# Performance work log

Hardware: AMD Instinct MI355X
Metric: run time of the kernel (lower is better)

Reference implementation:

```python
import jax, jax.numpy as jnp
import numpy as np

INITIAL_CAPITAL = 500.0
TRANSACTION_COST = 0.0003
TAU = 1.0  # gumbel-softmax temperature
B, S, F = 256, 4096, 64


def setup_inputs() -> dict:
    key = jax.random.key(0)
    ks = jax.random.split(key, 10)
    features = jax.random.normal(ks[0], (B, S, F), dtype=jnp.float32)
    # make columns 1/2 look like vix level / vix change so branches fire
    features = features.at[:, :, 1].set(20.0 + 10.0 * jax.random.uniform(ks[1], (B, S)))
    features = features.at[:, :, 2].set(0.5 * jax.random.normal(ks[2], (B, S)))
    features = features.at[:, :, 3].set(0.01 * jax.random.normal(ks[3], (B, S)))
    return {
        "features": features,
        "feature_weights": jnp.ones((F,), jnp.float32) / F,
        "long_threshold": jnp.float32(0.52),
        "short_threshold": jnp.float32(0.48),
        "base_position_size": jnp.float32(0.8),
        "conviction_scalar": jnp.float32(0.5),
        "vix_impact": jnp.float32(0.2),
        "vix_collapse_threshold": jnp.float32(0.15),
        "vix_spike_threshold": jnp.float32(0.15),
        "gumbel_noise": jax.random.gumbel(ks[4], (S, B, 3), dtype=jnp.float32),
    }


def reference(features, feature_weights, long_threshold, short_threshold,
              base_position_size, conviction_scalar, vix_impact,
              vix_collapse_threshold, vix_spike_threshold, gumbel_noise):
    batch, seq_len, _ = features.shape
    # predictions: sigmoid of feature-weighted sum  [B,S]
    predictions = jax.nn.sigmoid(jnp.einsum('bsf,f->bs', features, feature_weights))
    # time-major per-step inputs [S,B]
    pred_t = predictions.T
    mom_t = features[:, :, 0].T
    vix_t = features[:, :, 1].T
    vch_t = features[:, :, 2].T
    mret_t = features[:, :, 3].T

    def step(carry, x):
        eq, pos = carry  # eq [B], pos [B,3]
        p, v, dv, m, r, g = x
        signal_strength = jnp.abs(p - 0.5) / 0.5
        vix_collapse = (dv < -vix_collapse_threshold) & (v < 30.0)
        vix_spike = (dv > vix_spike_threshold) & (v > 20.0)
        psz = jnp.clip(base_position_size + conviction_scalar * signal_strength, 0.2, 1.0)
        psz = jnp.where(vix_collapse | vix_spike, psz * (1.0 + vix_impact), psz)
        long_pos = ((p >= long_threshold) & (m > 0)) | vix_collapse
        short_pos = ((p <= short_threshold) & (m < 0)) | vix_spike
        logits = jnp.stack([
            jnp.where(long_pos, 1.0, -10.0),
            jnp.where(short_pos, 1.0, -10.0),
            jnp.where(~long_pos & ~short_pos, 1.0, -10.0),
        ], axis=1)  # [B,3]
        probs = jax.nn.softmax((logits + g) / TAU, axis=1)
        strategy_return = psz * (probs[:, 0] - probs[:, 1]) * r
        position_change = jnp.abs(probs - pos).sum(axis=1)
        eq_new = eq * (1.0 + strategy_return - position_change * TRANSACTION_COST)
        return (eq_new, probs), (eq_new, probs, psz)

    eq0 = jnp.full((batch,), INITIAL_CAPITAL, dtype=features.dtype)
    pos0 = jnp.zeros((batch, 3), features.dtype).at[:, 2].set(1.0)
    (_, _), (eq_seq, pos_seq, psz_seq) = jax.lax.scan(
        step, (eq0, pos0), (pred_t, vix_t, vch_t, mom_t, mret_t, gumbel_noise))
    equity = jnp.concatenate([eq0[:, None], eq_seq.T], axis=1)          # [B,S+1]
    positions = jnp.concatenate([pos0[:, None], jnp.swapaxes(pos_seq, 0, 1)], axis=1)  # [B,S+1,3]
    position_sizes = psz_seq[-1]  # last timestep, matching torch loop leak
    return equity, positions, predictions, position_sizes
```

## Files before the change

kernel.cpp:

```cpp
#include <hip/hip_runtime.h>

#define Bn 256
#define Sn 4096
#define Fn 64
#define TCOST 0.0003f
#define INIT_CAP 500.0f

#define EQ_OFF   0
#define POS_OFF  (Bn * (Sn + 1))
#define PRED_OFF (Bn * (Sn + 1) * 4)
#define PSZ_OFF  (PRED_OFF + Bn * Sn)

#define ROWS_PB 64

__global__ __launch_bounds__(256) void trishot_fwd(
    const float* __restrict__ feat,
    const float* __restrict__ w,
    const float* __restrict__ p_lt, const float* __restrict__ p_st,
    const float* __restrict__ p_bps, const float* __restrict__ p_cs,
    const float* __restrict__ p_vi, const float* __restrict__ p_vct,
    const float* __restrict__ p_vst,
    const float* __restrict__ gumbel,
    float* __restrict__ out)
{
    const int tid  = threadIdx.x;
    const int lane = tid & 63;
    const int wave = tid >> 6;
    const int sub  = lane & 15;
    const int grp  = lane >> 4;

    const float LT = *p_lt, ST = *p_st, BPS = *p_bps, CS = *p_cs,
                VI = *p_vi, VCT = *p_vct, VST = *p_vst;

    const float4 wv = ((const float4*)w)[sub];

    const size_t r0 = (size_t)blockIdx.x * ROWS_PB;

#pragma unroll
    for (int pass = 0; pass < ROWS_PB / 16; ++pass) {
        const size_t row = r0 + (size_t)pass * 16 + (size_t)(wave * 4 + grp);
        const float4 fv = ((const float4*)feat)[row * 16 + sub];

        float x = fv.x * wv.x + fv.y * wv.y + fv.z * wv.z + fv.w * wv.w;
        x += __shfl_xor(x, 1);
        x += __shfl_xor(x, 2);
        x += __shfl_xor(x, 4);
        x += __shfl_xor(x, 8);

        if (sub == 0) {
            const int b = (int)(row >> 12);
            const int s = (int)(row & (Sn - 1));

            const float p = 1.0f / (1.0f + __expf(-x));
            const float mom = fv.x, vix = fv.y, dvix = fv.z, mret = fv.w;

            const float ss = fabsf(p - 0.5f) * 2.0f;
            const bool collapse = (dvix < -VCT) && (vix < 30.0f);
            const bool spike    = (dvix >  VST) && (vix > 20.0f);
            float psz = fminf(fmaxf(BPS + CS * ss, 0.2f), 1.0f);
            if (collapse || spike) psz *= (1.0f + VI);

            const bool lp = ((p >= LT) && (mom > 0.0f)) || collapse;
            const bool sp = ((p <= ST) && (mom < 0.0f)) || spike;
            const float l0 = lp ? 1.0f : -10.0f;
            const float l1 = sp ? 1.0f : -10.0f;
            const float l2 = (!lp && !sp) ? 1.0f : -10.0f;

            const float* g = gumbel + ((size_t)s * Bn + b) * 3;
            const float z0 = l0 + g[0], z1 = l1 + g[1], z2 = l2 + g[2];
            const float zm = fmaxf(z0, fmaxf(z1, z2));
            const float e0 = __expf(z0 - zm), e1 = __expf(z1 - zm),
                        e2 = __expf(z2 - zm);
            const float inv = 1.0f / (e0 + e1 + e2);
            const float q0 = e0 * inv, q1 = e1 * inv, q2 = e2 * inv;

            out[PRED_OFF + row] = p;

            const size_t prow = ((size_t)b * (Sn + 1) + s + 1) * 3;
            float* pos = out + POS_OFF;
            pos[prow + 0] = q0;
            pos[prow + 1] = q1;
            pos[prow + 2] = q2;

            out[EQ_OFF + (size_t)b * (Sn + 1) + s + 1] = psz * (q0 - q1) * mret;

            if (s == 0) {
                const size_t p0row = (size_t)b * (Sn + 1) * 3;
                pos[p0row + 0] = 0.0f;
                pos[p0row + 1] = 0.0f;
                pos[p0row + 2] = 1.0f;
            }
            if (s == Sn - 1) {
                out[PSZ_OFF + b] = psz;
            }
        }
    }
}

#define TB  512
#define CHB 8
#define PAD(i) ((i) + ((i) >> 4))

__global__ __launch_bounds__(TB) void trishot_scan(float* __restrict__ out)
{
    const int b = blockIdx.x;
    const int j = threadIdx.x;

    float* eq = out + EQ_OFF + (size_t)b * (Sn + 1);
    const float* pos = out + POS_OFF + (size_t)b * (Sn + 1) * 3;

    __shared__ float sfac[Sn + Sn / 16];
    __shared__ float sc[TB];

    for (int i = j; i < Sn; i += TB) {
        const float a0 = pos[(size_t)i * 3 + 0];
        const float a1 = pos[(size_t)i * 3 + 1];
        const float a2 = pos[(size_t)i * 3 + 2];
        const float c0 = pos[(size_t)(i + 1) * 3 + 0];
        const float c1 = pos[(size_t)(i + 1) * 3 + 1];
        const float c2 = pos[(size_t)(i + 1) * 3 + 2];
        const float pc = fabsf(c0 - a0) + fabsf(c1 - a1) + fabsf(c2 - a2);
        const float rp = eq[i + 1];
        sfac[PAD(i)] = 1.0f + rp - pc * TCOST;
    }
    __syncthreads();

    float f[CHB];
    float lprod = 1.0f;
    const int t0 = j * CHB;
#pragma unroll
    for (int i = 0; i < CHB; ++i) {
        const float v = sfac[PAD(t0 + i)];
        f[i] = v;
        lprod *= v;
    }
    sc[j] = lprod;
    __syncthreads();

#pragma unroll
    for (int off = 1; off < TB; off <<= 1) {
        const float mine  = sc[j];
        const float other = (j >= off) ? sc[j - off] : 1.0f;
        __syncthreads();
        sc[j] = mine * other;
        __syncthreads();
    }

    float eqv = INIT_CAP * ((j > 0) ? sc[j - 1] : 1.0f);
#pragma unroll
    for (int i = 0; i < CHB; ++i) {
        eqv *= f[i];
        sfac[PAD(t0 + i)] = eqv;
    }
    __syncthreads();
    for (int i = j; i < Sn; i += TB) {
        eq[i + 1] = sfac[PAD(i)];
    }
    if (j == 0) eq[0] = INIT_CAP;
}

extern "C" void kernel_launch(void* const* d_in, const int* in_sizes, int n_in,
                              void* d_out, int out_size, void* d_ws, size_t ws_size,
                              hipStream_t stream) {
    const float* feat   = (const float*)d_in[0];
    const float* w      = (const float*)d_in[1];
    const float* lt     = (const float*)d_in[2];
    const float* st     = (const float*)d_in[3];
    const float* bps    = (const float*)d_in[4];
    const float* cs     = (const float*)d_in[5];
    const float* vi     = (const float*)d_in[6];
    const float* vct    = (const float*)d_in[7];
    const float* vst    = (const float*)d_in[8];
    const float* gumbel = (const float*)d_in[9];
    float* out = (float*)d_out;

    trishot_fwd<<<(Bn * Sn) / ROWS_PB, 256, 0, stream>>>(
        feat, w, lt, st, bps, cs, vi, vct, vst, gumbel, out);
    trishot_scan<<<Bn, TB, 0, stream>>>(out);
}
```

Before: 391.3 us.

## Fuse forward pass and equity scan into one per-batch kernel via LDS

Merges the per-timestep forward kernel and the equity scan kernel into a single kernel with one 1024-thread block per batch row. Softmax probabilities and per-step returns are kept in LDS, so the scan no longer re-reads positions and returns from global memory, and one launch is removed. In exchange, the grid shrinks to one block per batch, which limits latency hiding for the feature stream, and equity writes become strided per thread.

```diff
diff --git a/kernel.cpp b/kernel.cpp
--- a/kernel.cpp
+++ b/kernel.cpp
@@ -11,9 +11,13 @@
 #define PRED_OFF (Bn * (Sn + 1) * 4)
 #define PSZ_OFF  (PRED_OFF + Bn * Sn)
 
-#define ROWS_PB 64
+#define TB   1024
+#define CHB  (Sn / TB)
+#define LQ   (Sn + 1)
+#define PADi(i) ((i) + ((i) >> 3))
+#define LQP  (LQ + (LQ >> 3) + 1)
 
-__global__ __launch_bounds__(256) void trishot_fwd(
+__global__ __launch_bounds__(TB) void trishot_fused(
     const float* __restrict__ feat,
     const float* __restrict__ w,
     const float* __restrict__ p_lt, const float* __restrict__ p_st,
@@ -23,22 +27,29 @@
     const float* __restrict__ gumbel,
     float* __restrict__ out)
 {
+    const int b    = blockIdx.x;
     const int tid  = threadIdx.x;
     const int lane = tid & 63;
-    const int wave = tid >> 6;
     const int sub  = lane & 15;
-    const int grp  = lane >> 4;
+    const int gid  = tid >> 4;
+
+    __shared__ float sq0[LQP];
+    __shared__ float sq1[LQP];
+    __shared__ float sq2[LQP];
+    __shared__ float srp[LQP];
+    __shared__ float sc[TB];
 
     const float LT = *p_lt, ST = *p_st, BPS = *p_bps, CS = *p_cs,
                 VI = *p_vi, VCT = *p_vct, VST = *p_vst;
 
     const float4 wv = ((const float4*)w)[sub];
 
-    const size_t r0 = (size_t)blockIdx.x * ROWS_PB;
+    float* pos = out + POS_OFF;
 
-#pragma unroll
-    for (int pass = 0; pass < ROWS_PB / 16; ++pass) {
-        const size_t row = r0 + (size_t)pass * 16 + (size_t)(wave * 4 + grp);
+#pragma unroll 4
+    for (int it = 0; it < Sn / (TB / 16); ++it) {
+        const int s = it * (TB / 16) + gid;
+        const size_t row = (size_t)b * Sn + s;
         const float4 fv = ((const float4*)feat)[row * 16 + sub];
 
         float x = fv.x * wv.x + fv.y * wv.y + fv.z * wv.z + fv.w * wv.w;
@@ -48,9 +59,6 @@
         x += __shfl_xor(x, 8);
 
         if (sub == 0) {
-            const int b = (int)(row >> 12);
-            const int s = (int)(row & (Sn - 1));
-
             const float p = 1.0f / (1.0f + __expf(-x));
             const float mom = fv.x, vix = fv.y, dvix = fv.z, mret = fv.w;
 
@@ -77,86 +85,70 @@
             out[PRED_OFF + row] = p;
 
             const size_t prow = ((size_t)b * (Sn + 1) + s + 1) * 3;
-            float* pos = out + POS_OFF;
             pos[prow + 0] = q0;
             pos[prow + 1] = q1;
             pos[prow + 2] = q2;
 
-            out[EQ_OFF + (size_t)b * (Sn + 1) + s + 1] = psz * (q0 - q1) * mret;
+            sq0[PADi(s + 1)] = q0;
+            sq1[PADi(s + 1)] = q1;
+            sq2[PADi(s + 1)] = q2;
+            srp[PADi(s + 1)] = psz * (q0 - q1) * mret;
 
-            if (s == 0) {
-                const size_t p0row = (size_t)b * (Sn + 1) * 3;
-                pos[p0row + 0] = 0.0f;
-                pos[p0row + 1] = 0.0f;
-                pos[p0row + 2] = 1.0f;
-            }
             if (s == Sn - 1) {
                 out[PSZ_OFF + b] = psz;
             }
         }
     }
-}
 
-#define TB  512
-#define CHB 8
-#define PAD(i) ((i) + ((i) >> 4))
-
-__global__ __launch_bounds__(TB) void trishot_scan(float* __restrict__ out)
-{
-    const int b = blockIdx.x;
-    const int j = threadIdx.x;
-
-    float* eq = out + EQ_OFF + (size_t)b * (Sn + 1);
-    const float* pos = out + POS_OFF + (size_t)b * (Sn + 1) * 3;
-
-    __shared__ float sfac[Sn + Sn / 16];
-    __shared__ float sc[TB];
-
-    for (int i = j; i < Sn; i += TB) {
-        const float a0 = pos[(size_t)i * 3 + 0];
-        const float a1 = pos[(size_t)i * 3 + 1];
-        const float a2 = pos[(size_t)i * 3 + 2];
-        const float c0 = pos[(size_t)(i + 1) * 3 + 0];
-        const float c1 = pos[(size_t)(i + 1) * 3 + 1];
-        const float c2 = pos[(size_t)(i + 1) * 3 + 2];
-        const float pc = fabsf(c0 - a0) + fabsf(c1 - a1) + fabsf(c2 - a2);
-        const float rp = eq[i + 1];
-        sfac[PAD(i)] = 1.0f + rp - pc * TCOST;
+    if (tid == 0) {
+        sq0[PADi(0)] = 0.0f;
+        sq1[PADi(0)] = 0.0f;
+        sq2[PADi(0)] = 1.0f;
+        const size_t p0row = (size_t)b * (Sn + 1) * 3;
+        pos[p0row + 0] = 0.0f;
+        pos[p0row + 1] = 0.0f;
+        pos[p0row + 2] = 1.0f;
+        out[EQ_OFF + (size_t)b * (Sn + 1)] = INIT_CAP;
     }
     __syncthreads();
 
+    const int t0 = tid * CHB;
+    float prev0 = sq0[PADi(t0)];
+    float prev1 = sq1[PADi(t0)];
+    float prev2 = sq2[PADi(t0)];
+
     float f[CHB];
     float lprod = 1.0f;
-    const int t0 = j * CHB;
 #pragma unroll
     for (int i = 0; i < CHB; ++i) {
-        const float v = sfac[PAD(t0 + i)];
-        f[i] = v;
-        lprod *= v;
+        const int s = t0 + i + 1;
+        const float c0 = sq0[PADi(s)], c1 = sq1[PADi(s)], c2 = sq2[PADi(s)];
+        const float pc = fabsf(c0 - prev0) + fabsf(c1 - prev1)
+                       + fabsf(c2 - prev2);
+        const float fac = 1.0f + srp[PADi(s)] - pc * TCOST;
+        f[i] = fac;
+        lprod *= fac;
+        prev0 = c0; prev1 = c1; prev2 = c2;
     }
-    sc[j] = lprod;
+    sc[tid] = lprod;
     __syncthreads();
 
 #pragma unroll
     for (int off = 1; off < TB; off <<= 1) {
-        const float mine  = sc[j];
-        const float other = (j >= off) ? sc[j - off] : 1.0f;
+        const float mine  = sc[tid];
+        const float other = (tid >= off) ? sc[tid - off] : 1.0f;
         __syncthreads();
-        sc[j] = mine * other;
+        sc[tid] = mine * other;
         __syncthreads();
     }
 
-    float eqv = INIT_CAP * ((j > 0) ? sc[j - 1] : 1.0f);
+    float* eq = out + EQ_OFF + (size_t)b * (Sn + 1);
+    float eqv = INIT_CAP * ((tid > 0) ? sc[tid - 1] : 1.0f);
 #pragma unroll
     for (int i = 0; i < CHB; ++i) {
         eqv *= f[i];
-        sfac[PAD(t0 + i)] = eqv;
+        eq[t0 + i + 1] = eqv;
     }
-    __syncthreads();
-    for (int i = j; i < Sn; i += TB) {
-        eq[i + 1] = sfac[PAD(i)];
-    }
-    if (j == 0) eq[0] = INIT_CAP;
 }
 
 extern "C" void kernel_launch(void* const* d_in, const int* in_sizes, int n_in,
@@ -174,7 +166,6 @@
     const float* gumbel = (const float*)d_in[9];
     float* out = (float*)d_out;
 
-    trishot_fwd<<<(Bn * Sn) / ROWS_PB, 256, 0, stream>>>(
+    trishot_fused<<<Bn, TB, 0, stream>>>(
         feat, w, lt, st, bps, cs, vi, vct, vst, gumbel, out);
-    trishot_scan<<<Bn, TB, 0, stream>>>(out);
 }
```

New measurement: 406.0 us. 3.8% more time.

## Replace shared-memory Hillis-Steele scan with wave-shuffle two-level product scan

Applied to the files above, without the earlier changes.

The per-batch cumulative product scan now uses 1024 threads with 4 elements each, doing an intra-wave shuffle scan followed by a small cross-wave scan over 16 wave totals. This replaces a 9-step shared-memory Hillis-Steele scan that needed two barriers per step. Results are written straight from registers to global memory instead of being staged back through shared memory. In exchange, the final stores are strided rather than coalesced, and the padding pattern used for the shared-memory stage changes.

```diff
diff --git a/kernel.cpp b/kernel.cpp
--- a/kernel.cpp
+++ b/kernel.cpp
@@ -97,65 +97,71 @@
     }
 }
 
-#define TB  512
-#define CHB 8
-#define PAD(i) ((i) + ((i) >> 4))
+#define TB   1024
+#define CHB  (Sn / TB)
+#define PADi(i) ((i) + ((i) >> 3))
 
 __global__ __launch_bounds__(TB) void trishot_scan(float* __restrict__ out)
 {
     const int b = blockIdx.x;
     const int j = threadIdx.x;
+    const int lane = j & 63;
+    const int wid  = j >> 6;
 
     float* eq = out + EQ_OFF + (size_t)b * (Sn + 1);
     const float* pos = out + POS_OFF + (size_t)b * (Sn + 1) * 3;
 
-    __shared__ float sfac[Sn + Sn / 16];
-    __shared__ float sc[TB];
+    __shared__ float sfac[Sn + (Sn >> 3)];
+    __shared__ float swave[16];
 
     for (int i = j; i < Sn; i += TB) {
-        const float a0 = pos[(size_t)i * 3 + 0];
-        const float a1 = pos[(size_t)i * 3 + 1];
-        const float a2 = pos[(size_t)i * 3 + 2];
-        const float c0 = pos[(size_t)(i + 1) * 3 + 0];
-        const float c1 = pos[(size_t)(i + 1) * 3 + 1];
-        const float c2 = pos[(size_t)(i + 1) * 3 + 2];
+        const float a0 = pos[i * 3 + 0];
+        const float a1 = pos[i * 3 + 1];
+        const float a2 = pos[i * 3 + 2];
+        const float c0 = pos[i * 3 + 3];
+        const float c1 = pos[i * 3 + 4];
+        const float c2 = pos[i * 3 + 5];
         const float pc = fabsf(c0 - a0) + fabsf(c1 - a1) + fabsf(c2 - a2);
         const float rp = eq[i + 1];
-        sfac[PAD(i)] = 1.0f + rp - pc * TCOST;
+        sfac[PADi(i)] = 1.0f + rp - pc * TCOST;
     }
     __syncthreads();
 
-    float f[CHB];
-    float lprod = 1.0f;
     const int t0 = j * CHB;
+    const float f0 = sfac[PADi(t0 + 0)];
+    const float f1 = sfac[PADi(t0 + 1)];
+    const float f2 = sfac[PADi(t0 + 2)];
+    const float f3 = sfac[PADi(t0 + 3)];
+    const float lprod = f0 * f1 * f2 * f3;
+
+    float incl = lprod;
 #pragma unroll
-    for (int i = 0; i < CHB; ++i) {
-        const float v = sfac[PAD(t0 + i)];
-        f[i] = v;
-        lprod *= v;
+    for (int off = 1; off < 64; off <<= 1) {
+        const float v = __shfl_up(incl, off);
+        if (lane >= off) incl *= v;
     }
-    sc[j] = lprod;
+    if (lane == 63) swave[wid] = incl;
     __syncthreads();
 
+    if (wid == 0) {
+        float wv = (lane < 16) ? swave[lane] : 1.0f;
 #pragma unroll
-    for (int off = 1; off < TB; off <<= 1) {
-        const float mine  = sc[j];
-        const float other = (j >= off) ? sc[j - off] : 1.0f;
-        __syncthreads();
-        sc[j] = mine * other;
-        __syncthreads();
-    }
-
-    float eqv = INIT_CAP * ((j > 0) ? sc[j - 1] : 1.0f);
-#pragma unroll
-    for (int i = 0; i < CHB; ++i) {
-        eqv *= f[i];
-        sfac[PAD(t0 + i)] = eqv;
+        for (int off = 1; off < 16; off <<= 1) {
+            const float v = __shfl_up(wv, off);
+            if (lane >= off) wv *= v;
+        }
+        if (lane < 16) swave[lane] = wv;
     }
     __syncthreads();
-    for (int i = j; i < Sn; i += TB) {
-        eq[i + 1] = sfac[PAD(i)];
-    }
+
+    const float woff = (wid > 0) ? swave[wid - 1] : 1.0f;
+    float excl = __shfl_up(incl, 1);
+    if (lane == 0) excl = 1.0f;
+    float eqv = INIT_CAP * woff * excl;
+    eqv *= f0; eq[t0 + 1] = eqv;
+    eqv *= f1; eq[t0 + 2] = eqv;
+    eqv *= f2; eq[t0 + 3] = eqv;
+    eqv *= f3; eq[t0 + 4] = eqv;
     if (j == 0) eq[0] = INIT_CAP;
 }
 
```

Result: no change. 388.1 us (-0.8%).
